# Performance work log

Measured on AMD Instinct MI355X. Metric: run time of the kernel, lower is better.

The kernel has to match this reference:

```python
import jax, jax.numpy as jnp
import numpy as np

NUM_NODES = 100000
NODE_DIM = 64
MEM_DIM = 64
EMBED = 64   # out_channels
HEADS = 2
IN_DIM = NODE_DIM + MEM_DIM  # 128
N = 50000    # batch nodes (len(n_id))
E = 800000   # edges in local subgraph


def setup_inputs() -> dict:
    key = jax.random.key(0)
    ks = jax.random.split(key, 12)
    s = 1.0 / np.sqrt(IN_DIM)
    inp = {
        "n_id": jax.random.randint(ks[0], (N,), 0, NUM_NODES),
        "edge_index": jax.random.randint(ks[1], (2, E), 0, N),
        # non-learned TGN memory state (detached in forward)
        "memory_table": jax.random.normal(ks[2], (NUM_NODES, MEM_DIM), jnp.float32),
        # learned node embedding table
        "emb_table": jax.random.normal(ks[3], (NUM_NODES, NODE_DIM), jnp.float32),
        # TransformerConv linear layers; weights stored [in, out] so y = x @ W + b
        "Wq": jax.random.normal(ks[4], (IN_DIM, HEADS * EMBED), jnp.float32) * s,
        "bq": jnp.zeros((HEADS * EMBED,), jnp.float32),
        "Wk": jax.random.normal(ks[5], (IN_DIM, HEADS * EMBED), jnp.float32) * s,
        "bk": jnp.zeros((HEADS * EMBED,), jnp.float32),
        "Wv": jax.random.normal(ks[6], (IN_DIM, HEADS * EMBED), jnp.float32) * s,
        "bv": jnp.zeros((HEADS * EMBED,), jnp.float32),
        "Wskip": jax.random.normal(ks[7], (IN_DIM, EMBED), jnp.float32) * s,
        "bskip": jnp.zeros((EMBED,), jnp.float32),
    }
    return inp


def reference(n_id, edge_index, memory_table, emb_table, Wq, bq, Wk, bk, Wv, bv, Wskip, bskip):
    # memory lookup (detached) + embedding lookup + concat([emb, mem])
    z = jax.lax.stop_gradient(memory_table[n_id])          # [N, MEM_DIM]
    x = jnp.concatenate([emb_table[n_id], z], axis=-1)     # [N, IN_DIM]

    q = (x @ Wq + bq).reshape(N, HEADS, EMBED)
    k = (x @ Wk + bk).reshape(N, HEADS, EMBED)
    v = (x @ Wv + bv).reshape(N, HEADS, EMBED)

    src, dst = edge_index[0], edge_index[1]
    # per-edge attention score: (q_i . k_j) / sqrt(d), i = dst, j = src
    score = jnp.einsum("ehd,ehd->eh", q[dst], k[src]) / np.sqrt(EMBED)  # [E, H]
    # scatter-softmax over incoming edges of each destination node
    smax = jax.ops.segment_max(score, dst, num_segments=N)              # [N, H]
    exps = jnp.exp(score - smax[dst])                                   # [E, H]
    denom = jax.ops.segment_sum(exps, dst, num_segments=N)              # [N, H]
    alpha = exps / denom[dst]                                           # [E, H]

    msg = alpha[:, :, None] * v[src]                                    # [E, H, D]
    out = jax.ops.segment_sum(msg, dst, num_segments=N)                 # [N, H, D]
    out = out.mean(axis=1)                                              # concat=False -> mean over heads
    out = out + x @ Wskip + bskip                                       # root_weight skip
    return out
```

## Files before the change

### kernel.cpp

```cpp
#include <hip/hip_runtime.h>
#include <math.h>


typedef unsigned int uint32;
typedef unsigned short ushort16;
typedef __attribute__((ext_vector_type(8))) short short8;
typedef __attribute__((ext_vector_type(4))) float floatx4;

__device__ __forceinline__ ushort16 f2bf(float f) {
  union { float f; uint32 u; } x; x.f = f;
  uint32 r = x.u + 0x7fffu + ((x.u >> 16) & 1u);
  return (ushort16)(r >> 16);
}
__device__ __forceinline__ float bf_lo(uint32 u) {
  union { uint32 u; float f; } x; x.u = u << 16; return x.f;
}
__device__ __forceinline__ float bf_hi(uint32 u) {
  union { uint32 u; float f; } x; x.u = u & 0xffff0000u; return x.f;
}
__device__ __forceinline__ void unpack8(uint4 u, float* f) {
  f[0] = bf_lo(u.x); f[1] = bf_hi(u.x); f[2] = bf_lo(u.y); f[3] = bf_hi(u.y);
  f[4] = bf_lo(u.z); f[5] = bf_hi(u.z); f[6] = bf_lo(u.w); f[7] = bf_hi(u.w);
}
__device__ __forceinline__ uint4 pack8(float4 a, float4 b) {
  uint4 r;
  r.x = (uint32)f2bf(a.x) | ((uint32)f2bf(a.y) << 16);
  r.y = (uint32)f2bf(a.z) | ((uint32)f2bf(a.w) << 16);
  r.z = (uint32)f2bf(b.x) | ((uint32)f2bf(b.y) << 16);
  r.w = (uint32)f2bf(b.z) | ((uint32)f2bf(b.w) << 16);
  return r;
}

__global__ __launch_bounds__(256) void prep_hist_kernel(
    const float* __restrict__ Wq, const float* __restrict__ bq,
    const float* __restrict__ Wk, const float* __restrict__ bk,
    const float* __restrict__ Wv, const float* __restrict__ bv,
    const float* __restrict__ Ws, const float* __restrict__ bs,
    ushort16* __restrict__ Wt, float* __restrict__ ball,
    const int* __restrict__ dstA, int E, int* __restrict__ counts) {
  int idx = blockIdx.x * 256 + threadIdx.x;
  if (idx < 448 * 128) {
    int n = idx >> 7, k = idx & 127;
    float w;
    if (n < 128)      w = Wq[k * 128 + n];
    else if (n < 256) w = Wk[k * 128 + (n - 128)];
    else if (n < 384) w = Wv[k * 128 + (n - 256)];
    else              w = Ws[k * 64 + (n - 384)];
    Wt[idx] = f2bf(w);
  }
  if (idx < 448) {
    float b;
    if (idx < 128)      b = bq[idx];
    else if (idx < 256) b = bk[idx - 128];
    else if (idx < 384) b = bv[idx - 256];
    else                b = bs[idx - 384];
    ball[idx] = b;
  }
  if (idx < E) atomicAdd(&counts[dstA[idx]], 1);
}

__global__ __launch_bounds__(256) void scan1_kernel(const int* __restrict__ counts,
                                                    int* __restrict__ offs,
                                                    int* __restrict__ bsum, int N) {
  __shared__ int s[256];
  int b = blockIdx.x, t = threadIdx.x;
  int base = b * 4096 + t * 16;
  int vals[16];
  int sum = 0;
#pragma unroll
  for (int i = 0; i < 16; ++i) {
    int idx = base + i;
    vals[i] = (idx < N) ? counts[idx] : 0;
    sum += vals[i];
  }
  s[t] = sum;
  __syncthreads();
  for (int off = 1; off < 256; off <<= 1) {
    int vv = (t >= off) ? s[t - off] : 0;
    __syncthreads();
    s[t] += vv;
    __syncthreads();
  }
  int run = (t > 0) ? s[t - 1] : 0;
#pragma unroll
  for (int i = 0; i < 16; ++i) {
    int idx = base + i;
    if (idx < N) offs[idx] = run;
    run += vals[i];
  }
  if (t == 255) bsum[b] = s[255];
}

__global__ __launch_bounds__(256) void scan3_kernel(int* __restrict__ offs,
                                                    const int* __restrict__ bsum,
                                                    int N, int E) {
  int i = blockIdx.x * blockDim.x + threadIdx.x;
  if (i < N) {
    int blk = i >> 12;
    int add = 0;
    for (int j = 0; j < blk; ++j) add += bsum[j];
    offs[i] += add;
  }
  if (i == 0) offs[N] = E;
}

__global__ __launch_bounds__(256) void scatter_kernel(
    const int* __restrict__ srcA, const int* __restrict__ dstA, int E,
    const int* __restrict__ offs, int* __restrict__ cursor,
    int* __restrict__ sorted_src) {
  int e = blockIdx.x * blockDim.x + threadIdx.x;
  if (e < E) {
    int d = dstA[e];
    int p = offs[d] + atomicAdd(&cursor[d], 1);
    sorted_src[p] = srcA[e];
  }
}

#define LDA 136
__global__ __launch_bounds__(256) void qkv_mfma_kernel(
    const int* __restrict__ n_id, const float* __restrict__ embtab,
    const float* __restrict__ memtab,
    const ushort16* __restrict__ Wt, const float* __restrict__ ball,
    ushort16* __restrict__ qb, ushort16* __restrict__ kb, ushort16* __restrict__ vb,
    float* __restrict__ outskip, int N) {
  __shared__ ushort16 As[128 * LDA];
  __shared__ ushort16 Bs[64 * LDA];
  int t = threadIdx.x;
  int row0 = blockIdx.x * 128;
  int ct = blockIdx.y;
  int col0 = ct * 64;

#pragma unroll
  for (int rep = 0; rep < 8; ++rep) {
    int idx = rep * 256 + t;
    int r = idx >> 4, c = idx & 15;
    int grow = row0 + r;
    uint4 outv = make_uint4(0u, 0u, 0u, 0u);
    if (grow < N) {
      int srcrow = n_id[grow];
      const float* srcp = (c < 8) ? (embtab + (size_t)srcrow * 64 + c * 8)
                                  : (memtab + (size_t)srcrow * 64 + (c - 8) * 8);
      float4 f0 = *(const float4*)srcp;
      float4 f1 = *(const float4*)(srcp + 4);
      outv = pack8(f0, f1);
    }
    *(uint4*)&As[r * LDA + c * 8] = outv;
  }
#pragma unroll
  for (int rep = 0; rep < 4; ++rep) {
    int idx = rep * 256 + t;
    int r = idx >> 4, c = idx & 15;
    uint4 val = *(const uint4*)(Wt + (size_t)(col0 + r) * 128 + c * 8);
    *(uint4*)&Bs[r * LDA + c * 8] = val;
  }
  __syncthreads();

  int wave = t >> 6, lane = t & 63;
  int m_base = wave * 32;
  int lrow = lane & 15, quad = lane >> 4;

  floatx4 acc[2][4];
#pragma unroll
  for (int i = 0; i < 2; ++i)
#pragma unroll
    for (int j = 0; j < 4; ++j) acc[i][j] = (floatx4)(0.f);

#pragma unroll
  for (int kk = 0; kk < 4; ++kk) {
    int koff = kk * 32 + quad * 8;
    short8 a0 = *(const short8*)&As[(m_base + lrow) * LDA + koff];
    short8 a1 = *(const short8*)&As[(m_base + 16 + lrow) * LDA + koff];
    short8 b0 = *(const short8*)&Bs[(lrow) * LDA + koff];
    short8 b1 = *(const short8*)&Bs[(16 + lrow) * LDA + koff];
    short8 b2 = *(const short8*)&Bs[(32 + lrow) * LDA + koff];
    short8 b3 = *(const short8*)&Bs[(48 + lrow) * LDA + koff];
    acc[0][0] = __builtin_amdgcn_mfma_f32_16x16x32_bf16(b0, a0, acc[0][0], 0, 0, 0);
    acc[0][1] = __builtin_amdgcn_mfma_f32_16x16x32_bf16(b1, a0, acc[0][1], 0, 0, 0);
    acc[0][2] = __builtin_amdgcn_mfma_f32_16x16x32_bf16(b2, a0, acc[0][2], 0, 0, 0);
    acc[0][3] = __builtin_amdgcn_mfma_f32_16x16x32_bf16(b3, a0, acc[0][3], 0, 0, 0);
    acc[1][0] = __builtin_amdgcn_mfma_f32_16x16x32_bf16(b0, a1, acc[1][0], 0, 0, 0);
    acc[1][1] = __builtin_amdgcn_mfma_f32_16x16x32_bf16(b1, a1, acc[1][1], 0, 0, 0);
    acc[1][2] = __builtin_amdgcn_mfma_f32_16x16x32_bf16(b2, a1, acc[1][2], 0, 0, 0);
    acc[1][3] = __builtin_amdgcn_mfma_f32_16x16x32_bf16(b3, a1, acc[1][3], 0, 0, 0);
  }

#pragma unroll
  for (int jt = 0; jt < 4; ++jt) {
    int gcol = col0 + jt * 16 + quad * 4;
    float4 bias = *(const float4*)(ball + gcol);
#pragma unroll
    for (int rt = 0; rt < 2; ++rt) {
      int grow = row0 + m_base + rt * 16 + lrow;
      if (grow >= N) continue;
      float o0 = acc[rt][jt][0] + bias.x;
      float o1 = acc[rt][jt][1] + bias.y;
      float o2 = acc[rt][jt][2] + bias.z;
      float o3 = acc[rt][jt][3] + bias.w;
      if (ct < 6) {
        uint2 pk;
        pk.x = (uint32)f2bf(o0) | ((uint32)f2bf(o1) << 16);
        pk.y = (uint32)f2bf(o2) | ((uint32)f2bf(o3) << 16);
        if (ct < 2)      *(uint2*)(qb + (size_t)grow * 128 + gcol)         = pk;
        else if (ct < 4) *(uint2*)(kb + (size_t)grow * 128 + (gcol - 128)) = pk;
        else             *(uint2*)(vb + (size_t)grow * 128 + (gcol - 256)) = pk;
      } else {
        *(float4*)(outskip + (size_t)grow * 64 + (gcol - 384)) =
            make_float4(o0, o1, o2, o3);
      }
    }
  }
}

#define EXPC 0.1803368801111244f
__global__ __launch_bounds__(256) void attn_kernel(
    const ushort16* __restrict__ qb, const ushort16* __restrict__ kb,
    const ushort16* __restrict__ vb, const int* __restrict__ offs,
    const int* __restrict__ ssrc, float* __restrict__ out, int N) {
  int tid = threadIdx.x;
  int wave = tid >> 6, lane = tid & 63;
  int nsub = lane >> 4;
  int l16 = lane & 15;
  int head = l16 >> 3;
  int l8 = lane & 7;
  int node = (blockIdx.x * 4 + wave) * 4 + nsub;
  bool valid = node < N;
  int nodeC = valid ? node : 0;

  int e0 = 0, e1 = 0;
  if (valid) { e0 = offs[node]; e1 = offs[node + 1]; }
  int deg = e1 - e0;
  int md = deg;
  md = max(md, __shfl_xor(md, 16));
  md = max(md, __shfl_xor(md, 32));

  int hoff = head * 64 + l8 * 8;
  float qf[8];
  {
    uint4 qu = *(const uint4*)(qb + (size_t)nodeC * 128 + hoff);
    unpack8(qu, qf);
  }

  float l = 0.f;
  float a[8];
#pragma unroll
  for (int j = 0; j < 8; ++j) a[j] = 0.f;

  uint4 k0v = make_uint4(0, 0, 0, 0), v0v = k0v, k1v = k0v, v1v = k0v;
  if (md > 0) {
    int e = e0;
    int s = (e < e1) ? ssrc[e] : 0;
    k0v = *(const uint4*)(kb + (size_t)s * 128 + hoff);
    v0v = *(const uint4*)(vb + (size_t)s * 128 + hoff);
  }
  if (md > 1) {
    int e = e0 + 1;
    int s = (e < e1) ? ssrc[e] : 0;
    k1v = *(const uint4*)(kb + (size_t)s * 128 + hoff);
    v1v = *(const uint4*)(vb + (size_t)s * 128 + hoff);
  }

  for (int i = 0; i < md; ++i) {
    uint4 kc = k0v, vc = v0v;
    k0v = k1v; v0v = v1v;
    if (i + 2 < md) {
      int e = e0 + i + 2;
      int s = (e < e1) ? ssrc[e] : 0;
      k1v = *(const uint4*)(kb + (size_t)s * 128 + hoff);
      v1v = *(const uint4*)(vb + (size_t)s * 128 + hoff);
    }
    float kf[8], vf[8];
    unpack8(kc, kf);
    unpack8(vc, vf);
    float p = qf[0] * kf[0];
#pragma unroll
    for (int j = 1; j < 8; ++j) p = fmaf(qf[j], kf[j], p);
    p += __shfl_xor(p, 1);
    p += __shfl_xor(p, 2);
    p += __shfl_xor(p, 4);
    float w = (i < deg) ? exp2f(p * EXPC) : 0.f;
    l += w;
#pragma unroll
    for (int j = 0; j < 8; ++j) a[j] = fmaf(w, vf[j], a[j]);
  }

  float inv = (l > 0.f) ? 0.5f / l : 0.f;
  float r[8];
#pragma unroll
  for (int j = 0; j < 8; ++j) r[j] = a[j] * inv;
#pragma unroll
  for (int j = 0; j < 8; ++j) r[j] += __shfl_xor(r[j], 8);

  if (valid && head == 0) {
    float* op = out + (size_t)node * 64 + l8 * 8;
    float4 c0 = *(float4*)op;
    float4 c1 = *(float4*)(op + 4);
    c0.x += r[0]; c0.y += r[1]; c0.z += r[2]; c0.w += r[3];
    c1.x += r[4]; c1.y += r[5]; c1.z += r[6]; c1.w += r[7];
    *(float4*)op = c0;
    *(float4*)(op + 4) = c1;
  }
}

extern "C" void kernel_launch(void* const* d_in, const int* in_sizes, int n_in,
                              void* d_out, int out_size, void* d_ws, size_t ws_size,
                              hipStream_t stream) {
  const int* n_id = (const int*)d_in[0];
  const int* eidx = (const int*)d_in[1];
  const float* memtab = (const float*)d_in[2];
  const float* embtab = (const float*)d_in[3];
  const float* Wq = (const float*)d_in[4];
  const float* bq = (const float*)d_in[5];
  const float* Wk = (const float*)d_in[6];
  const float* bk = (const float*)d_in[7];
  const float* Wv = (const float*)d_in[8];
  const float* bv = (const float*)d_in[9];
  const float* Wskip = (const float*)d_in[10];
  const float* bskip = (const float*)d_in[11];

  int N = in_sizes[0];
  int E = in_sizes[1] / 2;
  const int* srcA = eidx;
  const int* dstA = eidx + E;
  float* out = (float*)d_out;

  char* w = (char*)d_ws;
  ushort16* qb = (ushort16*)w; w += (size_t)N * 128 * 2;
  ushort16* kb = (ushort16*)w; w += (size_t)N * 128 * 2;
  ushort16* vb = (ushort16*)w; w += (size_t)N * 128 * 2;
  ushort16* Wt = (ushort16*)w; w += (size_t)448 * 128 * 2;
  float* ball = (float*)w;     w += (size_t)448 * 4;
  int* counts = (int*)w;       w += (size_t)N * 4;
  int* cursor = (int*)w;       w += (size_t)N * 4;
  int* offs = (int*)w;         w += (size_t)(N + 1) * 4;
  int* bsum = (int*)w;         w += (size_t)1024 * 4;
  int* ssrc = (int*)w;         w += (size_t)E * 4;

  hipMemsetAsync(counts, 0, (size_t)2 * N * 4, stream);

  int k1_threads = (448 * 128 > E) ? 448 * 128 : E;
  prep_hist_kernel<<<(k1_threads + 255) / 256, 256, 0, stream>>>(
      Wq, bq, Wk, bk, Wv, bv, Wskip, bskip, Wt, ball, dstA, E, counts);

  int NB = (N + 4095) / 4096;
  scan1_kernel<<<NB, 256, 0, stream>>>(counts, offs, bsum, N);
  scan3_kernel<<<(N + 255) / 256, 256, 0, stream>>>(offs, bsum, N, E);

  scatter_kernel<<<(E + 255) / 256, 256, 0, stream>>>(srcA, dstA, E, offs, cursor, ssrc);

  dim3 ggrid((N + 127) / 128, 7);
  qkv_mfma_kernel<<<ggrid, 256, 0, stream>>>(
      n_id, embtab, memtab, Wt, ball, qb, kb, vb, out, N);

  attn_kernel<<<(N + 15) / 16, 256, 0, stream>>>(qb, kb, vb, offs, ssrc, out, N);
}
```

Measured before the change: 309.2 us.

## Gather QKV inputs once per row and keep A fragments in registers

The QKV projection kernel stops using a 7-column-tile grid that re-gathered and re-packed the embedding and memory rows for every output tile. Each wave now loads its 16 rows once into MFMA A-fragments held in registers and loops over all 448 output columns, reading weight fragments straight from global memory (cached) with no shared memory or barrier. Separately, the scatter step seeds its cursor array with a device-to-device copy of the offsets, which drops one load per edge and halves the memset. The cost is more repeated global or L2 traffic for weights, and a longer serial loop per wave.

```diff
diff --git a/kernel.cpp b/kernel.cpp
--- a/kernel.cpp
+++ b/kernel.cpp
@@ -22,13 +22,13 @@
   f[0] = bf_lo(u.x); f[1] = bf_hi(u.x); f[2] = bf_lo(u.y); f[3] = bf_hi(u.y);
   f[4] = bf_lo(u.z); f[5] = bf_hi(u.z); f[6] = bf_lo(u.w); f[7] = bf_hi(u.w);
 }
-__device__ __forceinline__ uint4 pack8(float4 a, float4 b) {
-  uint4 r;
-  r.x = (uint32)f2bf(a.x) | ((uint32)f2bf(a.y) << 16);
-  r.y = (uint32)f2bf(a.z) | ((uint32)f2bf(a.w) << 16);
-  r.z = (uint32)f2bf(b.x) | ((uint32)f2bf(b.y) << 16);
-  r.w = (uint32)f2bf(b.z) | ((uint32)f2bf(b.w) << 16);
-  return r;
+__device__ __forceinline__ short8 pack8s(float4 a, float4 b) {
+  union { uint32 u[4]; short8 s; } r;
+  r.u[0] = (uint32)f2bf(a.x) | ((uint32)f2bf(a.y) << 16);
+  r.u[1] = (uint32)f2bf(a.z) | ((uint32)f2bf(a.w) << 16);
+  r.u[2] = (uint32)f2bf(b.x) | ((uint32)f2bf(b.y) << 16);
+  r.u[3] = (uint32)f2bf(b.z) | ((uint32)f2bf(b.w) << 16);
+  return r.s;
 }
 
 __global__ __launch_bounds__(256) void prep_hist_kernel(
@@ -106,106 +106,74 @@
 
 __global__ __launch_bounds__(256) void scatter_kernel(
     const int* __restrict__ srcA, const int* __restrict__ dstA, int E,
-    const int* __restrict__ offs, int* __restrict__ cursor,
-    int* __restrict__ sorted_src) {
+    int* __restrict__ cursor, int* __restrict__ sorted_src) {
   int e = blockIdx.x * blockDim.x + threadIdx.x;
   if (e < E) {
     int d = dstA[e];
-    int p = offs[d] + atomicAdd(&cursor[d], 1);
+    int p = atomicAdd(&cursor[d], 1);
     sorted_src[p] = srcA[e];
   }
 }
 
-#define LDA 136
-__global__ __launch_bounds__(256) void qkv_mfma_kernel(
+__global__ __launch_bounds__(256) void qkv_reg_kernel(
     const int* __restrict__ n_id, const float* __restrict__ embtab,
     const float* __restrict__ memtab,
     const ushort16* __restrict__ Wt, const float* __restrict__ ball,
     ushort16* __restrict__ qb, ushort16* __restrict__ kb, ushort16* __restrict__ vb,
     float* __restrict__ outskip, int N) {
-  __shared__ ushort16 As[128 * LDA];
-  __shared__ ushort16 Bs[64 * LDA];
   int t = threadIdx.x;
-  int row0 = blockIdx.x * 128;
-  int ct = blockIdx.y;
-  int col0 = ct * 64;
-
-#pragma unroll
-  for (int rep = 0; rep < 8; ++rep) {
-    int idx = rep * 256 + t;
-    int r = idx >> 4, c = idx & 15;
-    int grow = row0 + r;
-    uint4 outv = make_uint4(0u, 0u, 0u, 0u);
-    if (grow < N) {
-      int srcrow = n_id[grow];
-      const float* srcp = (c < 8) ? (embtab + (size_t)srcrow * 64 + c * 8)
-                                  : (memtab + (size_t)srcrow * 64 + (c - 8) * 8);
-      float4 f0 = *(const float4*)srcp;
-      float4 f1 = *(const float4*)(srcp + 4);
-      outv = pack8(f0, f1);
+  int wave = t >> 6, lane = t & 63;
+  int lrow = lane & 15, quad = lane >> 4;
+  int grow = blockIdx.x * 64 + wave * 16 + lrow;
+  bool rvalid = grow < N;
+  int srcrow = rvalid ? n_id[grow] : 0;
+
+  const float* embp = embtab + (size_t)srcrow * 64 + quad * 8;
+  const float* memp = memtab + (size_t)srcrow * 64 + quad * 8;
+  short8 af[4];
+  af[0] = pack8s(*(const float4*)(embp), *(const float4*)(embp + 4));
+  af[1] = pack8s(*(const float4*)(embp + 32), *(const float4*)(embp + 36));
+  af[2] = pack8s(*(const float4*)(memp), *(const float4*)(memp + 4));
+  af[3] = pack8s(*(const float4*)(memp + 32), *(const float4*)(memp + 36));
+
+  int bkoff = quad * 8;
+
+  for (int ct = 0; ct < 7; ++ct) {
+    int col0 = ct * 64;
+    floatx4 acc[4];
+#pragma unroll
+    for (int j = 0; j < 4; ++j) acc[j] = (floatx4)(0.f);
+
+#pragma unroll
+    for (int kk = 0; kk < 4; ++kk) {
+#pragma unroll
+      for (int jt = 0; jt < 4; ++jt) {
+        short8 bf = *(const short8*)(Wt + (size_t)(col0 + jt * 16 + lrow) * 128 +
+                                     kk * 32 + bkoff);
+        acc[jt] = __builtin_amdgcn_mfma_f32_16x16x32_bf16(bf, af[kk], acc[jt], 0, 0, 0);
+      }
     }
-    *(uint4*)&As[r * LDA + c * 8] = outv;
-  }
-#pragma unroll
-  for (int rep = 0; rep < 4; ++rep) {
-    int idx = rep * 256 + t;
-    int r = idx >> 4, c = idx & 15;
-    uint4 val = *(const uint4*)(Wt + (size_t)(col0 + r) * 128 + c * 8);
-    *(uint4*)&Bs[r * LDA + c * 8] = val;
-  }
-  __syncthreads();
-
-  int wave = t >> 6, lane = t & 63;
-  int m_base = wave * 32;
-  int lrow = lane & 15, quad = lane >> 4;
-
-  floatx4 acc[2][4];
-#pragma unroll
-  for (int i = 0; i < 2; ++i)
-#pragma unroll
-    for (int j = 0; j < 4; ++j) acc[i][j] = (floatx4)(0.f);
-
-#pragma unroll
-  for (int kk = 0; kk < 4; ++kk) {
-    int koff = kk * 32 + quad * 8;
-    short8 a0 = *(const short8*)&As[(m_base + lrow) * LDA + koff];
-    short8 a1 = *(const short8*)&As[(m_base + 16 + lrow) * LDA + koff];
-    short8 b0 = *(const short8*)&Bs[(lrow) * LDA + koff];
-    short8 b1 = *(const short8*)&Bs[(16 + lrow) * LDA + koff];
-    short8 b2 = *(const short8*)&Bs[(32 + lrow) * LDA + koff];
-    short8 b3 = *(const short8*)&Bs[(48 + lrow) * LDA + koff];
-    acc[0][0] = __builtin_amdgcn_mfma_f32_16x16x32_bf16(b0, a0, acc[0][0], 0, 0, 0);
-    acc[0][1] = __builtin_amdgcn_mfma_f32_16x16x32_bf16(b1, a0, acc[0][1], 0, 0, 0);
-    acc[0][2] = __builtin_amdgcn_mfma_f32_16x16x32_bf16(b2, a0, acc[0][2], 0, 0, 0);
-    acc[0][3] = __builtin_amdgcn_mfma_f32_16x16x32_bf16(b3, a0, acc[0][3], 0, 0, 0);
-    acc[1][0] = __builtin_amdgcn_mfma_f32_16x16x32_bf16(b0, a1, acc[1][0], 0, 0, 0);
-    acc[1][1] = __builtin_amdgcn_mfma_f32_16x16x32_bf16(b1, a1, acc[1][1], 0, 0, 0);
-    acc[1][2] = __builtin_amdgcn_mfma_f32_16x16x32_bf16(b2, a1, acc[1][2], 0, 0, 0);
-    acc[1][3] = __builtin_amdgcn_mfma_f32_16x16x32_bf16(b3, a1, acc[1][3], 0, 0, 0);
-  }
-
-#pragma unroll
-  for (int jt = 0; jt < 4; ++jt) {
-    int gcol = col0 + jt * 16 + quad * 4;
-    float4 bias = *(const float4*)(ball + gcol);
-#pragma unroll
-    for (int rt = 0; rt < 2; ++rt) {
-      int grow = row0 + m_base + rt * 16 + lrow;
-      if (grow >= N) continue;
-      float o0 = acc[rt][jt][0] + bias.x;
-      float o1 = acc[rt][jt][1] + bias.y;
-      float o2 = acc[rt][jt][2] + bias.z;
-      float o3 = acc[rt][jt][3] + bias.w;
-      if (ct < 6) {
-        uint2 pk;
-        pk.x = (uint32)f2bf(o0) | ((uint32)f2bf(o1) << 16);
-        pk.y = (uint32)f2bf(o2) | ((uint32)f2bf(o3) << 16);
-        if (ct < 2)      *(uint2*)(qb + (size_t)grow * 128 + gcol)         = pk;
-        else if (ct < 4) *(uint2*)(kb + (size_t)grow * 128 + (gcol - 128)) = pk;
-        else             *(uint2*)(vb + (size_t)grow * 128 + (gcol - 256)) = pk;
-      } else {
-        *(float4*)(outskip + (size_t)grow * 64 + (gcol - 384)) =
-            make_float4(o0, o1, o2, o3);
+
+    if (rvalid) {
+#pragma unroll
+      for (int jt = 0; jt < 4; ++jt) {
+        int gcol = col0 + jt * 16 + quad * 4;
+        float4 bias = *(const float4*)(ball + gcol);
+        float o0 = acc[jt][0] + bias.x;
+        float o1 = acc[jt][1] + bias.y;
+        float o2 = acc[jt][2] + bias.z;
+        float o3 = acc[jt][3] + bias.w;
+        if (ct < 6) {
+          uint2 pk;
+          pk.x = (uint32)f2bf(o0) | ((uint32)f2bf(o1) << 16);
+          pk.y = (uint32)f2bf(o2) | ((uint32)f2bf(o3) << 16);
+          if (ct < 2)      *(uint2*)(qb + (size_t)grow * 128 + gcol)         = pk;
+          else if (ct < 4) *(uint2*)(kb + (size_t)grow * 128 + (gcol - 128)) = pk;
+          else             *(uint2*)(vb + (size_t)grow * 128 + (gcol - 256)) = pk;
+        } else {
+          *(float4*)(outskip + (size_t)grow * 64 + (gcol - 384)) =
+              make_float4(o0, o1, o2, o3);
+        }
       }
     }
   }
@@ -335,7 +303,7 @@
   int* bsum = (int*)w;         w += (size_t)1024 * 4;
   int* ssrc = (int*)w;         w += (size_t)E * 4;
 
-  hipMemsetAsync(counts, 0, (size_t)2 * N * 4, stream);
+  hipMemsetAsync(counts, 0, (size_t)N * 4, stream);
 
   int k1_threads = (448 * 128 > E) ? 448 * 128 : E;
   prep_hist_kernel<<<(k1_threads + 255) / 256, 256, 0, stream>>>(
@@ -345,10 +313,11 @@
   scan1_kernel<<<NB, 256, 0, stream>>>(counts, offs, bsum, N);
   scan3_kernel<<<(N + 255) / 256, 256, 0, stream>>>(offs, bsum, N, E);
 
-  scatter_kernel<<<(E + 255) / 256, 256, 0, stream>>>(srcA, dstA, E, offs, cursor, ssrc);
-
-  dim3 ggrid((N + 127) / 128, 7);
-  qkv_mfma_kernel<<<ggrid, 256, 0, stream>>>(
+  hipMemcpyAsync(cursor, offs, (size_t)N * 4, hipMemcpyDeviceToDevice, stream);
+
+  scatter_kernel<<<(E + 255) / 256, 256, 0, stream>>>(srcA, dstA, E, cursor, ssrc);
+
+  qkv_reg_kernel<<<(N + 63) / 64, 256, 0, stream>>>(
       n_id, embtab, memtab, Wt, ball, qb, kb, vb, out, N);
 
   attn_kernel<<<(N + 15) / 16, 256, 0, stream>>>(qb, kb, vb, offs, ssrc, out, N);
```

Result: slower. 328.0 us (+6.1%).
